# Kernel optimization log

Measured on AMD Instinct MI355X. Metric: run time of the kernel, lower is better.

Reference implementation:

```python
import jax, jax.numpy as jnp
import numpy as np

B, N_MM, N_V, N_A = 2, 256, 64, 128
DIM, HEADS, ATTN_RATIO, MLP_RATIO = 1024, 16, 0.25, 4.0
INNER = int(DIM * ATTN_RATIO)          # 256
HID = int(DIM * MLP_RATIO)             # 4096
SCALE = (DIM // HEADS) ** -0.5         # faithful to source: uses dim//num_heads
EPS = 1e-5


def setup_inputs() -> dict:
    key = jax.random.key(0)
    ks = jax.random.split(key, 16)
    s = 0.02
    return {
        "xmm": jax.random.normal(ks[0], (B, N_MM, DIM), jnp.float32),
        "xv": jax.random.normal(ks[1], (B, N_V, DIM), jnp.float32),
        "xa": jax.random.normal(ks[2], (B, N_A, DIM), jnp.float32),
        "ln_mm_w": jnp.ones((DIM,), jnp.float32),
        "ln_mm_b": jnp.zeros((DIM,), jnp.float32),
        "ln_v_w": jnp.ones((DIM,), jnp.float32),
        "ln_v_b": jnp.zeros((DIM,), jnp.float32),
        "ln_a_w": jnp.ones((DIM,), jnp.float32),
        "ln_a_b": jnp.zeros((DIM,), jnp.float32),
        "Wq": jax.random.normal(ks[3], (DIM, INNER), jnp.float32) * s,
        "Wkv": jax.random.normal(ks[4], (2 * DIM, 2 * INNER), jnp.float32) * s,
        "Wproj": jax.random.normal(ks[5], (INNER, DIM), jnp.float32) * s,
        "bproj": jnp.zeros((DIM,), jnp.float32),
        "ln_mlp_w": jnp.ones((DIM,), jnp.float32),
        "ln_mlp_b": jnp.zeros((DIM,), jnp.float32),
        "W1": jax.random.normal(ks[6], (DIM, HID), jnp.float32) * s,
        "b1": jnp.zeros((HID,), jnp.float32),
        "W2": jax.random.normal(ks[7], (HID, DIM), jnp.float32) * s,
        "b2": jnp.zeros((DIM,), jnp.float32),
    }


def _ln(x, w, b):
    m = x.mean(-1, keepdims=True)
    v = ((x - m) ** 2).mean(-1, keepdims=True)
    return (x - m) / jnp.sqrt(v + EPS) * w + b


def reference(xmm, xv, xa, ln_mm_w, ln_mm_b, ln_v_w, ln_v_b, ln_a_w, ln_a_b,
              Wq, Wkv, Wproj, bproj, ln_mlp_w, ln_mlp_b, W1, b1, W2, b2):
    hd = INNER // HEADS
    src_mm = _ln(xmm, ln_mm_w, ln_mm_b)
    src_v = _ln(xv, ln_v_w, ln_v_b)
    src_a = _ln(xa, ln_a_w, ln_a_b)

    # kv(x_va) where x_va = cat([xv broadcast over N_a, xa broadcast over N_v], -1).
    # Equivalent to projecting each stream separately and broadcast-adding:
    kv_v = src_v @ Wkv[:DIM]            # [B, N_v, 2*INNER]
    kv_a = src_a @ Wkv[DIM:]            # [B, N_a, 2*INNER]
    kv = kv_v[:, :, None, :] + kv_a[:, None, :, :]          # [B, N_v, N_a, 2*INNER]
    kv = kv.reshape(B, N_V * N_A, 2, HEADS, hd)
    k = kv[:, :, 0].transpose(0, 2, 1, 3)                   # [B, H, N_va, hd]
    v = kv[:, :, 1].transpose(0, 2, 1, 3)

    q = (src_mm @ Wq).reshape(B, N_MM, HEADS, hd).transpose(0, 2, 1, 3)

    attn = jnp.einsum('bhqd,bhkd->bhqk', q, k) * SCALE
    attn = jax.nn.softmax(attn, axis=-1)
    out = jnp.einsum('bhqk,bhkd->bhqd', attn, v)
    out = out.transpose(0, 2, 1, 3).reshape(B, N_MM, INNER)
    out = out @ Wproj + bproj

    xmm = xmm + out
    h = _ln(xmm, ln_mlp_w, ln_mlp_b)
    h = jax.nn.gelu(h @ W1 + b1, approximate=False) @ W2 + b2
    return xmm + h
```

## Files before the change

kernel.cpp:

```cpp
#include <hip/hip_runtime.h>
#include <hip/hip_bf16.h>
#include <math.h>


typedef unsigned short ushort_t;
typedef __attribute__((ext_vector_type(8))) __bf16 bf16x8;
typedef __attribute__((ext_vector_type(4))) float f32x4;

#define DEVFN static __device__ __forceinline__

DEVFN float bf2f(ushort_t u) {
    return __uint_as_float(((unsigned int)u) << 16);
}
DEVFN ushort_t f2bf(float f) {
    unsigned int x = __float_as_uint(f);
    unsigned int r = x + 0x7FFFu + ((x >> 16) & 1u);
    return (ushort_t)(r >> 16);
}
DEVFN void unpack8(uint4 dv, float* dst) {
    unsigned int ws[4] = {dv.x, dv.y, dv.z, dv.w};
#pragma unroll
    for (int i = 0; i < 4; i++) {
        dst[2 * i] = __uint_as_float(ws[i] << 16);
        dst[2 * i + 1] = __uint_as_float(ws[i] & 0xFFFF0000u);
    }
}

struct LNSeg {
    const float* x; const float* w; const float* b; ushort_t* out; int start;
};
struct TDesc { const float* in; ushort_t* out; int R, C, nx, start; };

__global__ __launch_bounds__(256) void prep_kernel(LNSeg l0, LNSeg l1,
                                                   LNSeg l2, TDesc d0,
                                                   TDesc d1, TDesc d2,
                                                   TDesc d3, TDesc d4,
                                                   float* stats) {
    int id = blockIdx.x;
    int tid = threadIdx.x;
    if (id == 0) ((float4*)stats)[tid] = (float4){0.f, 0.f, 0.f, 0.f};

    if (id < 896) {
        const float *x, *w, *b; ushort_t* o; int start;
        if (id >= l2.start)      { x = l2.x; w = l2.w; b = l2.b; o = l2.out; start = l2.start; }
        else if (id >= l1.start) { x = l1.x; w = l1.w; b = l1.b; o = l1.out; start = l1.start; }
        else                     { x = l0.x; w = l0.w; b = l0.b; o = l0.out; start = 0; }
        int row = id - start;
        const float4* xr4 = (const float4*)(x + (size_t)row * 1024);
        float4 v4 = xr4[tid];
        float s = v4.x + v4.y + v4.z + v4.w;
        float ss = v4.x * v4.x + v4.y * v4.y + v4.z * v4.z + v4.w * v4.w;
#pragma unroll
        for (int off = 32; off > 0; off >>= 1) {
            s += __shfl_down(s, off);
            ss += __shfl_down(ss, off);
        }
        __shared__ float red[8];
        if ((tid & 63) == 0) {
            red[tid >> 6] = s;
            red[4 + (tid >> 6)] = ss;
        }
        __syncthreads();
        s = red[0] + red[1] + red[2] + red[3];
        ss = red[4] + red[5] + red[6] + red[7];
        float mean = s * (1.f / 1024.f);
        float var = ss * (1.f / 1024.f) - mean * mean;
        float rstd = rsqrtf(var + 1e-5f);
        const float4 w4 = ((const float4*)w)[tid];
        const float4 b4 = ((const float4*)b)[tid];
        union { ushort_t u[4]; uint2 v; } pk;
        pk.u[0] = f2bf((v4.x - mean) * rstd * w4.x + b4.x);
        pk.u[1] = f2bf((v4.y - mean) * rstd * w4.y + b4.y);
        pk.u[2] = f2bf((v4.z - mean) * rstd * w4.z + b4.z);
        pk.u[3] = f2bf((v4.w - mean) * rstd * w4.w + b4.w);
        *(uint2*)(o + (size_t)row * 1024 + tid * 4) = pk.v;
        return;
    }

    int t = id - 896;
    const float* in; ushort_t* out; int R, C, nx, start;
    if (t >= d4.start)      { in = d4.in; out = d4.out; R = d4.R; C = d4.C; nx = d4.nx; start = d4.start; }
    else if (t >= d3.start) { in = d3.in; out = d3.out; R = d3.R; C = d3.C; nx = d3.nx; start = d3.start; }
    else if (t >= d2.start) { in = d2.in; out = d2.out; R = d2.R; C = d2.C; nx = d2.nx; start = d2.start; }
    else if (t >= d1.start) { in = d1.in; out = d1.out; R = d1.R; C = d1.C; nx = d1.nx; start = d1.start; }
    else                    { in = d0.in; out = d0.out; R = d0.R; C = d0.C; nx = d0.nx; start = 0; }
    int tt = t - start;
    int bx = (tt % nx) * 32;
    int by = (tt / nx) * 32;
    __shared__ ushort_t tile[32 * 33];
    int r = tid >> 3, c4 = (tid & 7) * 4;
    float4 f = *(const float4*)(in + (size_t)(by + r) * C + bx + c4);
    ushort_t* tr = tile + r * 33 + c4;
    tr[0] = f2bf(f.x); tr[1] = f2bf(f.y); tr[2] = f2bf(f.z); tr[3] = f2bf(f.w);
    __syncthreads();
    int oc = tid >> 3, or4 = (tid & 7) * 4;
    union { ushort_t u[4]; uint2 v; } pk;
#pragma unroll
    for (int j = 0; j < 4; j++) pk.u[j] = tile[(or4 + j) * 33 + oc];
    *(uint2*)(out + (size_t)(bx + oc) * R + by + or4) = pk.v;
}

DEVFN void gemm64_item(const ushort_t* __restrict__ A, int lda,
                       const ushort_t* __restrict__ B, int ldb,
                       ushort_t* __restrict__ C, int ldc, int K, int m0,
                       int n0, ushort_t* As, ushort_t* Bs) {
    constexpr int LS = 40;
    int tid = threadIdx.x;
    int wave = tid >> 6, lane = tid & 63;
    int wm = wave >> 1, wn = wave & 1;
    int quad = lane >> 4, l16 = lane & 15;

    f32x4 acc[2][2];
#pragma unroll
    for (int i = 0; i < 2; i++)
#pragma unroll
        for (int j = 0; j < 2; j++) acc[i][j] = (f32x4){0.f, 0.f, 0.f, 0.f};

    int r = tid >> 2, c = tid & 3;
    const ushort_t* Ap = A + (size_t)(m0 + r) * lda + c * 8;
    const ushort_t* Bp = B + (size_t)(n0 + r) * ldb + c * 8;
    uint4 ra = *(const uint4*)Ap;
    uint4 rb = *(const uint4*)Bp;

    for (int k0 = 0; k0 < K; k0 += 32) {
        *(uint4*)(&As[r * LS + c * 8]) = ra;
        *(uint4*)(&Bs[r * LS + c * 8]) = rb;
        __syncthreads();
        if (k0 + 32 < K) {
            ra = *(const uint4*)(Ap + k0 + 32);
            rb = *(const uint4*)(Bp + k0 + 32);
        }
        bf16x8 af[2], bfr[2];
#pragma unroll
        for (int i = 0; i < 2; i++)
            af[i] = *(const bf16x8*)(&As[(wm * 32 + i * 16 + l16) * LS + quad * 8]);
#pragma unroll
        for (int j = 0; j < 2; j++)
            bfr[j] = *(const bf16x8*)(&Bs[(wn * 32 + j * 16 + l16) * LS + quad * 8]);
#pragma unroll
        for (int i = 0; i < 2; i++)
#pragma unroll
            for (int j = 0; j < 2; j++)
                acc[i][j] = __builtin_amdgcn_mfma_f32_16x16x32_bf16(
                    af[i], bfr[j], acc[i][j], 0, 0, 0);
        __syncthreads();
    }

#pragma unroll
    for (int i = 0; i < 2; i++)
#pragma unroll
        for (int j = 0; j < 2; j++) {
            int col = n0 + wn * 32 + j * 16 + l16;
            int rbase = m0 + wm * 32 + i * 16 + quad * 4;
#pragma unroll
            for (int rr = 0; rr < 4; rr++)
                C[(size_t)(rbase + rr) * ldc + col] = f2bf(acc[i][j][rr]);
        }
}

struct GSeg {
    const ushort_t* A; const ushort_t* B; ushort_t* C;
    int lda, ldb, ldc, nx, start;
};
__global__ __launch_bounds__(256) void gemm64_multi(GSeg s0, GSeg s1, GSeg s2,
                                                    int K) {
    __shared__ ushort_t As[64 * 40];
    __shared__ ushort_t Bs[64 * 40];
    int id = blockIdx.x;
    GSeg s = (id >= s2.start) ? s2 : ((id >= s1.start) ? s1 : s0);
    int t = id - s.start;
    gemm64_item(s.A, s.lda, s.B, s.ldb, s.C, s.ldc, K, (t / s.nx) * 64,
                (t % s.nx) * 64, As, Bs);
}

template <int EPI, typename OutT>
DEVFN void gemm128_core(const ushort_t* __restrict__ A, int lda,
                        const ushort_t* __restrict__ B, int ldb,
                        OutT* __restrict__ C, int ldc,
                        const float* __restrict__ bias, int K, int m0, int n0,
                        ushort_t* As, ushort_t* Bs) {
    constexpr int LS = 40;
    int tid = threadIdx.x;
    int wave = tid >> 6, lane = tid & 63;
    int wm = wave >> 1, wn = wave & 1;
    int quad = lane >> 4, l16 = lane & 15;

    f32x4 acc[4][4];
#pragma unroll
    for (int i = 0; i < 4; i++)
#pragma unroll
        for (int j = 0; j < 4; j++) acc[i][j] = (f32x4){0.f, 0.f, 0.f, 0.f};

    int r = tid >> 1;
    int c = (tid & 1) * 16;
    const ushort_t* Ap = A + (size_t)(m0 + r) * lda + c;
    const ushort_t* Bp = B + (size_t)(n0 + r) * ldb + c;
    uint4 ra0 = *(const uint4*)Ap;
    uint4 ra1 = *(const uint4*)(Ap + 8);
    uint4 rb0 = *(const uint4*)Bp;
    uint4 rb1 = *(const uint4*)(Bp + 8);

    for (int k0 = 0; k0 < K; k0 += 32) {
        *(uint4*)(&As[r * LS + c]) = ra0;
        *(uint4*)(&As[r * LS + c + 8]) = ra1;
        *(uint4*)(&Bs[r * LS + c]) = rb0;
        *(uint4*)(&Bs[r * LS + c + 8]) = rb1;
        __syncthreads();
        if (k0 + 32 < K) {
            ra0 = *(const uint4*)(Ap + k0 + 32);
            ra1 = *(const uint4*)(Ap + k0 + 40);
            rb0 = *(const uint4*)(Bp + k0 + 32);
            rb1 = *(const uint4*)(Bp + k0 + 40);
        }
        bf16x8 af[4], bfr[4];
#pragma unroll
        for (int i = 0; i < 4; i++)
            af[i] = *(const bf16x8*)(&As[(wm * 64 + i * 16 + l16) * LS + quad * 8]);
#pragma unroll
        for (int j = 0; j < 4; j++)
            bfr[j] = *(const bf16x8*)(&Bs[(wn * 64 + j * 16 + l16) * LS + quad * 8]);
#pragma unroll
        for (int i = 0; i < 4; i++)
#pragma unroll
            for (int j = 0; j < 4; j++)
                acc[i][j] = __builtin_amdgcn_mfma_f32_16x16x32_bf16(
                    af[i], bfr[j], acc[i][j], 0, 0, 0);
        __syncthreads();
    }

#pragma unroll
    for (int i = 0; i < 4; i++)
#pragma unroll
        for (int j = 0; j < 4; j++) {
            int col = n0 + wn * 64 + j * 16 + l16;
            int rbase = m0 + wm * 64 + i * 16 + quad * 4;
            float bv = (EPI == 2) ? bias[col] : 0.f;
#pragma unroll
            for (int rr = 0; rr < 4; rr++) {
                int row = rbase + rr;
                float vv = acc[i][j][rr] + bv;
                if constexpr (EPI == 2) {
                    vv = 0.5f * vv * (1.f + erff(vv * 0.70710678118654752f));
                    C[(size_t)row * ldc + col] = (OutT)f2bf(vv);
                } else {
                    atomicAdd((float*)&C[(size_t)row * ldc + col], vv);
                }
            }
        }
}

__global__ __launch_bounds__(256) void gemm_mlp1(
    const ushort_t* __restrict__ h0, const ushort_t* __restrict__ W1t,
    const float* __restrict__ b1, ushort_t* __restrict__ g) {
    __shared__ ushort_t As[128 * 40];
    __shared__ ushort_t Bs[128 * 40];
    gemm128_core<2, ushort_t>(h0, 1024, W1t, 1024, g, 4096, b1, 1024,
                              blockIdx.y * 128, blockIdx.x * 128, As, Bs);
}

__global__ __launch_bounds__(256) void gemm_mlp2(
    const ushort_t* __restrict__ g, const ushort_t* __restrict__ W2t,
    float* __restrict__ outp) {
    __shared__ ushort_t As[128 * 40];
    __shared__ ushort_t Bs[128 * 40];
    int z = blockIdx.z;
    gemm128_core<5, float>(g + z * 512, 4096, W2t + z * 512, 4096, outp, 1024,
                           nullptr, 512, blockIdx.y * 128, blockIdx.x * 128,
                           As, Bs);
}

__global__ __launch_bounds__(256) void gemm_proj(
    const ushort_t* __restrict__ A, const ushort_t* __restrict__ Bt,
    const float* __restrict__ bproj, const float* __restrict__ xmm,
    const float* __restrict__ b2, float* __restrict__ y,
    float* __restrict__ outp, float* __restrict__ stats) {
    constexpr int LS = 40;
    __shared__ ushort_t As[64 * LS];
    __shared__ ushort_t Bs[64 * LS];
    int tid = threadIdx.x;
    int wave = tid >> 6, lane = tid & 63;
    int wm = wave >> 1, wn = wave & 1;
    int quad = lane >> 4, l16 = lane & 15;
    int m0 = blockIdx.y * 64, n0 = blockIdx.x * 64;

    f32x4 acc[2][2];
#pragma unroll
    for (int i = 0; i < 2; i++)
#pragma unroll
        for (int j = 0; j < 2; j++) acc[i][j] = (f32x4){0.f, 0.f, 0.f, 0.f};

    int r = tid >> 2, c = tid & 3;
    const ushort_t* Ap = A + (size_t)(m0 + r) * 256 + c * 8;
    const ushort_t* Bp = Bt + (size_t)(n0 + r) * 256 + c * 8;
    uint4 ra = *(const uint4*)Ap;
    uint4 rb = *(const uint4*)Bp;

    for (int k0 = 0; k0 < 256; k0 += 32) {
        *(uint4*)(&As[r * LS + c * 8]) = ra;
        *(uint4*)(&Bs[r * LS + c * 8]) = rb;
        __syncthreads();
        if (k0 + 32 < 256) {
            ra = *(const uint4*)(Ap + k0 + 32);
            rb = *(const uint4*)(Bp + k0 + 32);
        }
        bf16x8 af[2], bfr[2];
#pragma unroll
        for (int i = 0; i < 2; i++)
            af[i] = *(const bf16x8*)(&As[(wm * 32 + i * 16 + l16) * LS + quad * 8]);
#pragma unroll
        for (int j = 0; j < 2; j++)
            bfr[j] = *(const bf16x8*)(&Bs[(wn * 32 + j * 16 + l16) * LS + quad * 8]);
#pragma unroll
        for (int i = 0; i < 2; i++)
#pragma unroll
            for (int j = 0; j < 2; j++)
                acc[i][j] = __builtin_amdgcn_mfma_f32_16x16x32_bf16(
                    af[i], bfr[j], acc[i][j], 0, 0, 0);
        __syncthreads();
    }

    float rs[2][4] = {{0.f, 0.f, 0.f, 0.f}, {0.f, 0.f, 0.f, 0.f}};
    float rq[2][4] = {{0.f, 0.f, 0.f, 0.f}, {0.f, 0.f, 0.f, 0.f}};
#pragma unroll
    for (int i = 0; i < 2; i++)
#pragma unroll
        for (int j = 0; j < 2; j++) {
            int col = n0 + wn * 32 + j * 16 + l16;
            int rbase = m0 + wm * 32 + i * 16 + quad * 4;
            float bv = bproj[col];
            float b2v = b2[col];
#pragma unroll
            for (int rr = 0; rr < 4; rr++) {
                int row = rbase + rr;
                float vv = acc[i][j][rr] + bv + xmm[(size_t)row * 1024 + col];
                y[(size_t)row * 1024 + col] = vv;
                outp[(size_t)row * 1024 + col] = vv + b2v;
                rs[i][rr] += vv;
                rq[i][rr] += vv * vv;
            }
        }
#pragma unroll
    for (int i = 0; i < 2; i++)
#pragma unroll
        for (int rr = 0; rr < 4; rr++) {
            float s = rs[i][rr], q = rq[i][rr];
            s += __shfl_xor(s, 1); q += __shfl_xor(q, 1);
            s += __shfl_xor(s, 2); q += __shfl_xor(q, 2);
            s += __shfl_xor(s, 4); q += __shfl_xor(q, 4);
            s += __shfl_xor(s, 8); q += __shfl_xor(q, 8);
            if (l16 == 0) {
                int row = m0 + wm * 32 + i * 16 + quad * 4 + rr;
                atomicAdd(&stats[row], s);
                atomicAdd(&stats[512 + row], q);
            }
        }
}

__global__ __launch_bounds__(256) void ln_apply(
    const float* __restrict__ y, const float* __restrict__ stats,
    const float* __restrict__ w, const float* __restrict__ b,
    ushort_t* __restrict__ h0) {
    int row = blockIdx.x, tid = threadIdx.x;
    float s = stats[row], ss = stats[512 + row];
    float mean = s * (1.f / 1024.f);
    float rstd = rsqrtf(ss * (1.f / 1024.f) - mean * mean + 1e-5f);
    float4 v4 = ((const float4*)(y + (size_t)row * 1024))[tid];
    float4 w4 = ((const float4*)w)[tid];
    float4 b4 = ((const float4*)b)[tid];
    union { ushort_t u[4]; uint2 v; } pk;
    pk.u[0] = f2bf((v4.x - mean) * rstd * w4.x + b4.x);
    pk.u[1] = f2bf((v4.y - mean) * rstd * w4.y + b4.y);
    pk.u[2] = f2bf((v4.z - mean) * rstd * w4.z + b4.z);
    pk.u[3] = f2bf((v4.w - mean) * rstd * w4.w + b4.w);
    *(uint2*)(h0 + (size_t)row * 1024 + tid * 4) = pk.v;
}

__global__ __launch_bounds__(256) void attn_kernel(
    const ushort_t* __restrict__ q, const ushort_t* __restrict__ kvv,
    const ushort_t* __restrict__ kva, ushort_t* __restrict__ out) {
    int bh = blockIdx.x;
    int b = bh >> 4, h = bh & 15;
    int tid = threadIdx.x;

    __shared__ float Kv[64][16], Vv[64][16], Ka[128][16], Va[128][16];
    {
        int row = tid >> 2, seg = (tid >> 1) & 1, half = tid & 1;
        const ushort_t* src =
            kvv + (size_t)(b * 64 + row) * 512 + seg * 256 + h * 16 + half * 8;
        float* dst = (seg ? Vv[row] : Kv[row]) + half * 8;
        unpack8(*(const uint4*)src, dst);
    }
#pragma unroll
    for (int t2 = 0; t2 < 2; t2++) {
        int t = tid + t2 * 256;
        int row = t >> 2, seg = (t >> 1) & 1, half = t & 1;
        const ushort_t* src =
            kva + (size_t)(b * 128 + row) * 512 + seg * 256 + h * 16 + half * 8;
        float* dst = (seg ? Va[row] : Ka[row]) + half * 8;
        unpack8(*(const uint4*)src, dst);
    }
    __syncthreads();

    int qlocal = tid >> 2;
    int dg = tid & 3;
    int qrow = blockIdx.y * 64 + qlocal;
    const ushort_t* qp = q + (size_t)(b * 256 + qrow) * 256 + h * 16 + dg * 4;
    uint2 qu = *(const uint2*)qp;
    float4 qv;
    qv.x = __uint_as_float(qu.x << 16) * 0.125f;
    qv.y = __uint_as_float(qu.x & 0xFFFF0000u) * 0.125f;
    qv.z = __uint_as_float(qu.y << 16) * 0.125f;
    qv.w = __uint_as_float(qu.y & 0xFFFF0000u) * 0.125f;

    const float4* Kv4 = (const float4*)Kv;
    const float4* Vv4 = (const float4*)Vv;
    const float4* Ka4 = (const float4*)Ka;
    const float4* Va4 = (const float4*)Va;

    float4 ov = {0.f, 0.f, 0.f, 0.f};
    float den = 0.f;
#pragma unroll 8
    for (int i = 0; i < 64; i++) {
        float4 kk = Kv4[i * 4 + dg];
        float part = qv.x * kk.x + qv.y * kk.y + qv.z * kk.z + qv.w * kk.w;
        part += __shfl_xor(part, 1);
        part += __shfl_xor(part, 2);
        float pe = __expf(part);
        den += pe;
        float4 vv = Vv4[i * 4 + dg];
        ov.x += pe * vv.x; ov.y += pe * vv.y;
        ov.z += pe * vv.z; ov.w += pe * vv.w;
    }
    float4 oa = {0.f, 0.f, 0.f, 0.f};
    float dena = 0.f;
#pragma unroll 8
    for (int i = 0; i < 128; i++) {
        float4 kk = Ka4[i * 4 + dg];
        float part = qv.x * kk.x + qv.y * kk.y + qv.z * kk.z + qv.w * kk.w;
        part += __shfl_xor(part, 1);
        part += __shfl_xor(part, 2);
        float pe = __expf(part);
        dena += pe;
        float4 vv = Va4[i * 4 + dg];
        oa.x += pe * vv.x; oa.y += pe * vv.y;
        oa.z += pe * vv.z; oa.w += pe * vv.w;
    }

    float rv = 1.f / den, ra = 1.f / dena;
    union { ushort_t u[4]; uint2 v; } pk;
    pk.u[0] = f2bf(ov.x * rv + oa.x * ra);
    pk.u[1] = f2bf(ov.y * rv + oa.y * ra);
    pk.u[2] = f2bf(ov.z * rv + oa.z * ra);
    pk.u[3] = f2bf(ov.w * rv + oa.w * ra);
    *(uint2*)(out + (size_t)(b * 256 + qrow) * 256 + h * 16 + dg * 4) = pk.v;
}

extern "C" void kernel_launch(void* const* d_in, const int* in_sizes, int n_in,
                              void* d_out, int out_size, void* d_ws,
                              size_t ws_size, hipStream_t stream) {
    const float* xmm = (const float*)d_in[0];
    const float* xv = (const float*)d_in[1];
    const float* xa = (const float*)d_in[2];
    const float* ln_mm_w = (const float*)d_in[3];
    const float* ln_mm_b = (const float*)d_in[4];
    const float* ln_v_w = (const float*)d_in[5];
    const float* ln_v_b = (const float*)d_in[6];
    const float* ln_a_w = (const float*)d_in[7];
    const float* ln_a_b = (const float*)d_in[8];
    const float* Wq = (const float*)d_in[9];
    const float* Wkv = (const float*)d_in[10];
    const float* Wproj = (const float*)d_in[11];
    const float* bproj = (const float*)d_in[12];
    const float* ln_mlp_w = (const float*)d_in[13];
    const float* ln_mlp_b = (const float*)d_in[14];
    const float* W1 = (const float*)d_in[15];
    const float* b1 = (const float*)d_in[16];
    const float* W2 = (const float*)d_in[17];
    const float* b2 = (const float*)d_in[18];
    float* outp = (float*)d_out;

    char* w = (char*)d_ws;
    ushort_t* xmmN = (ushort_t*)w;    w += 512 * 1024 * 2;
    ushort_t* xvN = (ushort_t*)w;     w += 128 * 1024 * 2;
    ushort_t* xaN = (ushort_t*)w;     w += 256 * 1024 * 2;
    ushort_t* Wqt = (ushort_t*)w;     w += 256 * 1024 * 2;
    ushort_t* Wkvt = (ushort_t*)w;    w += 512 * 2048 * 2;
    ushort_t* Wprojt = (ushort_t*)w;  w += 1024 * 256 * 2;
    ushort_t* W1t = (ushort_t*)w;     w += 4096 * 1024 * 2;
    ushort_t* W2t = (ushort_t*)w;     w += 1024 * 4096 * 2;
    ushort_t* qout = (ushort_t*)w;    w += 512 * 256 * 2;
    ushort_t* kvvb = (ushort_t*)w;    w += 128 * 512 * 2;
    ushort_t* kvab = (ushort_t*)w;    w += 256 * 512 * 2;
    ushort_t* attnout = (ushort_t*)w; w += 512 * 256 * 2;
    float* y = (float*)w;             w += 512 * 1024 * 4;
    ushort_t* h0 = (ushort_t*)w;      w += 512 * 1024 * 2;
    ushort_t* g = (ushort_t*)w;       w += 512 * 4096 * 2;
    float* stats = (float*)w;         w += 1024 * 4;

    LNSeg L0{xmm, ln_mm_w, ln_mm_b, xmmN, 0};
    LNSeg L1{xv, ln_v_w, ln_v_b, xvN, 512};
    LNSeg L2{xa, ln_a_w, ln_a_b, xaN, 640};
    TDesc T0{Wq, Wqt, 1024, 256, 8, 0};
    TDesc T1{Wkv, Wkvt, 2048, 512, 16, 256};
    TDesc T2{Wproj, Wprojt, 256, 1024, 32, 1280};
    TDesc T3{W1, W1t, 1024, 4096, 128, 1536};
    TDesc T4{W2, W2t, 4096, 1024, 32, 5632};
    prep_kernel<<<896 + 9728, 256, 0, stream>>>(L0, L1, L2, T0, T1, T2, T3,
                                                T4, stats);

    GSeg G0{xmmN, Wqt, qout, 1024, 1024, 256, 4, 0};
    GSeg G1{xvN, Wkvt, kvvb, 1024, 2048, 512, 8, 32};
    GSeg G2{xaN, Wkvt + 1024, kvab, 1024, 2048, 512, 8, 48};
    gemm64_multi<<<80, 256, 0, stream>>>(G0, G1, G2, 1024);

    attn_kernel<<<dim3(32, 4), 256, 0, stream>>>(qout, kvvb, kvab, attnout);

    gemm_proj<<<dim3(16, 8), 256, 0, stream>>>(attnout, Wprojt, bproj, xmm,
                                               b2, y, outp, stats);

    ln_apply<<<512, 256, 0, stream>>>(y, stats, ln_mlp_w, ln_mlp_b, h0);

    gemm_mlp1<<<dim3(32, 4), 256, 0, stream>>>(h0, W1t, b1, g);

    gemm_mlp2<<<dim3(8, 4, 8), 256, 0, stream>>>(g, W2t, outp);

    (void)in_sizes; (void)n_in; (void)out_size; (void)ws_size;
}
```

Before: 213.9 us.

## Replace LDS-staged GEMMs with single-wave register-direct MFMA tiles

All GEMMs (qkv, proj, mlp1, mlp2) now run as one-wave blocks that load MFMA operand fragments straight from global memory into registers, with a register double buffer and no shared memory or barriers. The grids change to match: more, smaller blocks, and mlp2 uses a 4-way K split instead of 8-way. The weight transpose in the prep kernel moves from 32x32 to 64x64 tiles, so it launches far fewer blocks. The aim is to cut LDS traffic and sync overhead and raise block counts. The cost is that each wave re-reads operands from global and L2 with no sharing inside a block.

After: 207.6 us. -3.0%, faster.

```diff
diff --git a/kernel.cpp b/kernel.cpp
--- a/kernel.cpp
+++ b/kernel.cpp
@@ -17,6 +17,11 @@
     unsigned int r = x + 0x7FFFu + ((x >> 16) & 1u);
     return (ushort_t)(r >> 16);
 }
+DEVFN bf16x8 asbf8(uint4 v) {
+    union { uint4 u; bf16x8 b; } c;
+    c.u = v;
+    return c.b;
+}
 DEVFN void unpack8(uint4 dv, float* dst) {
     unsigned int ws[4] = {dv.x, dv.y, dv.z, dv.w};
 #pragma unroll
@@ -26,307 +31,116 @@
     }
 }
 
-struct LNSeg {
-    const float* x; const float* w; const float* b; ushort_t* out; int start;
-};
-struct TDesc { const float* in; ushort_t* out; int R, C, nx, start; };
-
-__global__ __launch_bounds__(256) void prep_kernel(LNSeg l0, LNSeg l1,
-                                                   LNSeg l2, TDesc d0,
-                                                   TDesc d1, TDesc d2,
-                                                   TDesc d3, TDesc d4,
-                                                   float* stats) {
+template <int TM, int K>
+DEVFN void wave_acc(const ushort_t* __restrict__ A, int lda,
+                    const ushort_t* __restrict__ B, int ldb, int m0, int n0,
+                    int lane, f32x4 (&acc)[TM][4]) {
+    int quad = lane >> 4, l16 = lane & 15;
+    const ushort_t* Ap = A + (size_t)(m0 + l16) * lda + quad * 8;
+    const ushort_t* Bp = B + (size_t)(n0 + l16) * ldb + quad * 8;
+
+    uint4 ra[TM], rb[4];
+#pragma unroll
+    for (int i = 0; i < TM; i++)
+        ra[i] = *(const uint4*)(Ap + (size_t)i * 16 * lda);
+#pragma unroll
+    for (int j = 0; j < 4; j++)
+        rb[j] = *(const uint4*)(Bp + (size_t)j * 16 * ldb);
+
+#pragma unroll 2
+    for (int k0 = 0; k0 < K; k0 += 32) {
+        uint4 na[TM], nb[4];
+        if (k0 + 32 < K) {
+#pragma unroll
+            for (int i = 0; i < TM; i++)
+                na[i] = *(const uint4*)(Ap + (size_t)i * 16 * lda + k0 + 32);
+#pragma unroll
+            for (int j = 0; j < 4; j++)
+                nb[j] = *(const uint4*)(Bp + (size_t)j * 16 * ldb + k0 + 32);
+        }
+#pragma unroll
+        for (int i = 0; i < TM; i++) {
+            bf16x8 af = asbf8(ra[i]);
+#pragma unroll
+            for (int j = 0; j < 4; j++)
+                acc[i][j] = __builtin_amdgcn_mfma_f32_16x16x32_bf16(
+                    af, asbf8(rb[j]), acc[i][j], 0, 0, 0);
+        }
+        if (k0 + 32 < K) {
+#pragma unroll
+            for (int i = 0; i < TM; i++) ra[i] = na[i];
+#pragma unroll
+            for (int j = 0; j < 4; j++) rb[j] = nb[j];
+        }
+    }
+}
+
+__global__ __launch_bounds__(64) void qkv_kernel(
+    const ushort_t* __restrict__ xmmN, const ushort_t* __restrict__ xvN,
+    const ushort_t* __restrict__ xaN, const ushort_t* __restrict__ Wqt,
+    const ushort_t* __restrict__ Wkvt, ushort_t* __restrict__ qout,
+    ushort_t* __restrict__ kvvb, ushort_t* __restrict__ kvab) {
     int id = blockIdx.x;
-    int tid = threadIdx.x;
-    if (id == 0) ((float4*)stats)[tid] = (float4){0.f, 0.f, 0.f, 0.f};
-
-    if (id < 896) {
-        const float *x, *w, *b; ushort_t* o; int start;
-        if (id >= l2.start)      { x = l2.x; w = l2.w; b = l2.b; o = l2.out; start = l2.start; }
-        else if (id >= l1.start) { x = l1.x; w = l1.w; b = l1.b; o = l1.out; start = l1.start; }
-        else                     { x = l0.x; w = l0.w; b = l0.b; o = l0.out; start = 0; }
-        int row = id - start;
-        const float4* xr4 = (const float4*)(x + (size_t)row * 1024);
-        float4 v4 = xr4[tid];
-        float s = v4.x + v4.y + v4.z + v4.w;
-        float ss = v4.x * v4.x + v4.y * v4.y + v4.z * v4.z + v4.w * v4.w;
-#pragma unroll
-        for (int off = 32; off > 0; off >>= 1) {
-            s += __shfl_down(s, off);
-            ss += __shfl_down(ss, off);
-        }
-        __shared__ float red[8];
-        if ((tid & 63) == 0) {
-            red[tid >> 6] = s;
-            red[4 + (tid >> 6)] = ss;
-        }
-        __syncthreads();
-        s = red[0] + red[1] + red[2] + red[3];
-        ss = red[4] + red[5] + red[6] + red[7];
-        float mean = s * (1.f / 1024.f);
-        float var = ss * (1.f / 1024.f) - mean * mean;
-        float rstd = rsqrtf(var + 1e-5f);
-        const float4 w4 = ((const float4*)w)[tid];
-        const float4 b4 = ((const float4*)b)[tid];
-        union { ushort_t u[4]; uint2 v; } pk;
-        pk.u[0] = f2bf((v4.x - mean) * rstd * w4.x + b4.x);
-        pk.u[1] = f2bf((v4.y - mean) * rstd * w4.y + b4.y);
-        pk.u[2] = f2bf((v4.z - mean) * rstd * w4.z + b4.z);
-        pk.u[3] = f2bf((v4.w - mean) * rstd * w4.w + b4.w);
-        *(uint2*)(o + (size_t)row * 1024 + tid * 4) = pk.v;
-        return;
-    }
-
-    int t = id - 896;
-    const float* in; ushort_t* out; int R, C, nx, start;
-    if (t >= d4.start)      { in = d4.in; out = d4.out; R = d4.R; C = d4.C; nx = d4.nx; start = d4.start; }
-    else if (t >= d3.start) { in = d3.in; out = d3.out; R = d3.R; C = d3.C; nx = d3.nx; start = d3.start; }
-    else if (t >= d2.start) { in = d2.in; out = d2.out; R = d2.R; C = d2.C; nx = d2.nx; start = d2.start; }
-    else if (t >= d1.start) { in = d1.in; out = d1.out; R = d1.R; C = d1.C; nx = d1.nx; start = d1.start; }
-    else                    { in = d0.in; out = d0.out; R = d0.R; C = d0.C; nx = d0.nx; start = 0; }
-    int tt = t - start;
-    int bx = (tt % nx) * 32;
-    int by = (tt / nx) * 32;
-    __shared__ ushort_t tile[32 * 33];
-    int r = tid >> 3, c4 = (tid & 7) * 4;
-    float4 f = *(const float4*)(in + (size_t)(by + r) * C + bx + c4);
-    ushort_t* tr = tile + r * 33 + c4;
-    tr[0] = f2bf(f.x); tr[1] = f2bf(f.y); tr[2] = f2bf(f.z); tr[3] = f2bf(f.w);
-    __syncthreads();
-    int oc = tid >> 3, or4 = (tid & 7) * 4;
-    union { ushort_t u[4]; uint2 v; } pk;
-#pragma unroll
-    for (int j = 0; j < 4; j++) pk.u[j] = tile[(or4 + j) * 33 + oc];
-    *(uint2*)(out + (size_t)(bx + oc) * R + by + or4) = pk.v;
-}
-
-DEVFN void gemm64_item(const ushort_t* __restrict__ A, int lda,
-                       const ushort_t* __restrict__ B, int ldb,
-                       ushort_t* __restrict__ C, int ldc, int K, int m0,
-                       int n0, ushort_t* As, ushort_t* Bs) {
-    constexpr int LS = 40;
-    int tid = threadIdx.x;
-    int wave = tid >> 6, lane = tid & 63;
-    int wm = wave >> 1, wn = wave & 1;
+    int lane = threadIdx.x;
+    const ushort_t *A, *B;
+    ushort_t* C;
+    int lda, ldb, ldc, m0, n0;
+    if (id < 64) {
+        A = xmmN; B = Wqt; C = qout; lda = 1024; ldb = 1024; ldc = 256;
+        m0 = (id >> 2) * 32; n0 = (id & 3) * 64;
+    } else if (id < 96) {
+        int t = id - 64;
+        A = xvN; B = Wkvt; C = kvvb; lda = 1024; ldb = 2048; ldc = 512;
+        m0 = (t >> 3) * 32; n0 = (t & 7) * 64;
+    } else {
+        int t = id - 96;
+        A = xaN; B = Wkvt + 1024; C = kvab; lda = 1024; ldb = 2048; ldc = 512;
+        m0 = (t >> 3) * 32; n0 = (t & 7) * 64;
+    }
+    f32x4 acc[2][4];
+#pragma unroll
+    for (int i = 0; i < 2; i++)
+#pragma unroll
+        for (int j = 0; j < 4; j++) acc[i][j] = (f32x4){0.f, 0.f, 0.f, 0.f};
+    wave_acc<2, 1024>(A, lda, B, ldb, m0, n0, lane, acc);
+
     int quad = lane >> 4, l16 = lane & 15;
-
-    f32x4 acc[2][2];
 #pragma unroll
     for (int i = 0; i < 2; i++)
 #pragma unroll
-        for (int j = 0; j < 2; j++) acc[i][j] = (f32x4){0.f, 0.f, 0.f, 0.f};
-
-    int r = tid >> 2, c = tid & 3;
-    const ushort_t* Ap = A + (size_t)(m0 + r) * lda + c * 8;
-    const ushort_t* Bp = B + (size_t)(n0 + r) * ldb + c * 8;
-    uint4 ra = *(const uint4*)Ap;
-    uint4 rb = *(const uint4*)Bp;
-
-    for (int k0 = 0; k0 < K; k0 += 32) {
-        *(uint4*)(&As[r * LS + c * 8]) = ra;
-        *(uint4*)(&Bs[r * LS + c * 8]) = rb;
-        __syncthreads();
-        if (k0 + 32 < K) {
-            ra = *(const uint4*)(Ap + k0 + 32);
-            rb = *(const uint4*)(Bp + k0 + 32);
-        }
-        bf16x8 af[2], bfr[2];
-#pragma unroll
-        for (int i = 0; i < 2; i++)
-            af[i] = *(const bf16x8*)(&As[(wm * 32 + i * 16 + l16) * LS + quad * 8]);
-#pragma unroll
-        for (int j = 0; j < 2; j++)
-            bfr[j] = *(const bf16x8*)(&Bs[(wn * 32 + j * 16 + l16) * LS + quad * 8]);
-#pragma unroll
-        for (int i = 0; i < 2; i++)
-#pragma unroll
-            for (int j = 0; j < 2; j++)
-                acc[i][j] = __builtin_amdgcn_mfma_f32_16x16x32_bf16(
-                    af[i], bfr[j], acc[i][j], 0, 0, 0);
-        __syncthreads();
-    }
-
-#pragma unroll
-    for (int i = 0; i < 2; i++)
-#pragma unroll
-        for (int j = 0; j < 2; j++) {
-            int col = n0 + wn * 32 + j * 16 + l16;
-            int rbase = m0 + wm * 32 + i * 16 + quad * 4;
+        for (int j = 0; j < 4; j++) {
+            int col = n0 + j * 16 + l16;
+            int rbase = m0 + i * 16 + quad * 4;
 #pragma unroll
             for (int rr = 0; rr < 4; rr++)
                 C[(size_t)(rbase + rr) * ldc + col] = f2bf(acc[i][j][rr]);
         }
 }
 
-struct GSeg {
-    const ushort_t* A; const ushort_t* B; ushort_t* C;
-    int lda, ldb, ldc, nx, start;
-};
-__global__ __launch_bounds__(256) void gemm64_multi(GSeg s0, GSeg s1, GSeg s2,
-                                                    int K) {
-    __shared__ ushort_t As[64 * 40];
-    __shared__ ushort_t Bs[64 * 40];
-    int id = blockIdx.x;
-    GSeg s = (id >= s2.start) ? s2 : ((id >= s1.start) ? s1 : s0);
-    int t = id - s.start;
-    gemm64_item(s.A, s.lda, s.B, s.ldb, s.C, s.ldc, K, (t / s.nx) * 64,
-                (t % s.nx) * 64, As, Bs);
-}
-
-template <int EPI, typename OutT>
-DEVFN void gemm128_core(const ushort_t* __restrict__ A, int lda,
-                        const ushort_t* __restrict__ B, int ldb,
-                        OutT* __restrict__ C, int ldc,
-                        const float* __restrict__ bias, int K, int m0, int n0,
-                        ushort_t* As, ushort_t* Bs) {
-    constexpr int LS = 40;
-    int tid = threadIdx.x;
-    int wave = tid >> 6, lane = tid & 63;
-    int wm = wave >> 1, wn = wave & 1;
-    int quad = lane >> 4, l16 = lane & 15;
-
-    f32x4 acc[4][4];
-#pragma unroll
-    for (int i = 0; i < 4; i++)
-#pragma unroll
-        for (int j = 0; j < 4; j++) acc[i][j] = (f32x4){0.f, 0.f, 0.f, 0.f};
-
-    int r = tid >> 1;
-    int c = (tid & 1) * 16;
-    const ushort_t* Ap = A + (size_t)(m0 + r) * lda + c;
-    const ushort_t* Bp = B + (size_t)(n0 + r) * ldb + c;
-    uint4 ra0 = *(const uint4*)Ap;
-    uint4 ra1 = *(const uint4*)(Ap + 8);
-    uint4 rb0 = *(const uint4*)Bp;
-    uint4 rb1 = *(const uint4*)(Bp + 8);
-
-    for (int k0 = 0; k0 < K; k0 += 32) {
-        *(uint4*)(&As[r * LS + c]) = ra0;
-        *(uint4*)(&As[r * LS + c + 8]) = ra1;
-        *(uint4*)(&Bs[r * LS + c]) = rb0;
-        *(uint4*)(&Bs[r * LS + c + 8]) = rb1;
-        __syncthreads();
-        if (k0 + 32 < K) {
-            ra0 = *(const uint4*)(Ap + k0 + 32);
-            ra1 = *(const uint4*)(Ap + k0 + 40);
-            rb0 = *(const uint4*)(Bp + k0 + 32);
-            rb1 = *(const uint4*)(Bp + k0 + 40);
-        }
-        bf16x8 af[4], bfr[4];
-#pragma unroll
-        for (int i = 0; i < 4; i++)
-            af[i] = *(const bf16x8*)(&As[(wm * 64 + i * 16 + l16) * LS + quad * 8]);
-#pragma unroll
-        for (int j = 0; j < 4; j++)
-            bfr[j] = *(const bf16x8*)(&Bs[(wn * 64 + j * 16 + l16) * LS + quad * 8]);
-#pragma unroll
-        for (int i = 0; i < 4; i++)
-#pragma unroll
-            for (int j = 0; j < 4; j++)
-                acc[i][j] = __builtin_amdgcn_mfma_f32_16x16x32_bf16(
-                    af[i], bfr[j], acc[i][j], 0, 0, 0);
-        __syncthreads();
-    }
-
-#pragma unroll
-    for (int i = 0; i < 4; i++)
-#pragma unroll
-        for (int j = 0; j < 4; j++) {
-            int col = n0 + wn * 64 + j * 16 + l16;
-            int rbase = m0 + wm * 64 + i * 16 + quad * 4;
-            float bv = (EPI == 2) ? bias[col] : 0.f;
-#pragma unroll
-            for (int rr = 0; rr < 4; rr++) {
-                int row = rbase + rr;
-                float vv = acc[i][j][rr] + bv;
-                if constexpr (EPI == 2) {
-                    vv = 0.5f * vv * (1.f + erff(vv * 0.70710678118654752f));
-                    C[(size_t)row * ldc + col] = (OutT)f2bf(vv);
-                } else {
-                    atomicAdd((float*)&C[(size_t)row * ldc + col], vv);
-                }
-            }
-        }
-}
-
-__global__ __launch_bounds__(256) void gemm_mlp1(
-    const ushort_t* __restrict__ h0, const ushort_t* __restrict__ W1t,
-    const float* __restrict__ b1, ushort_t* __restrict__ g) {
-    __shared__ ushort_t As[128 * 40];
-    __shared__ ushort_t Bs[128 * 40];
-    gemm128_core<2, ushort_t>(h0, 1024, W1t, 1024, g, 4096, b1, 1024,
-                              blockIdx.y * 128, blockIdx.x * 128, As, Bs);
-}
-
-__global__ __launch_bounds__(256) void gemm_mlp2(
-    const ushort_t* __restrict__ g, const ushort_t* __restrict__ W2t,
-    float* __restrict__ outp) {
-    __shared__ ushort_t As[128 * 40];
-    __shared__ ushort_t Bs[128 * 40];
-    int z = blockIdx.z;
-    gemm128_core<5, float>(g + z * 512, 4096, W2t + z * 512, 4096, outp, 1024,
-                           nullptr, 512, blockIdx.y * 128, blockIdx.x * 128,
-                           As, Bs);
-}
-
-__global__ __launch_bounds__(256) void gemm_proj(
-    const ushort_t* __restrict__ A, const ushort_t* __restrict__ Bt,
+__global__ __launch_bounds__(64) void proj_kernel(
+    const ushort_t* __restrict__ attnout, const ushort_t* __restrict__ Wprojt,
     const float* __restrict__ bproj, const float* __restrict__ xmm,
     const float* __restrict__ b2, float* __restrict__ y,
     float* __restrict__ outp, float* __restrict__ stats) {
-    constexpr int LS = 40;
-    __shared__ ushort_t As[64 * LS];
-    __shared__ ushort_t Bs[64 * LS];
-    int tid = threadIdx.x;
-    int wave = tid >> 6, lane = tid & 63;
-    int wm = wave >> 1, wn = wave & 1;
+    int id = blockIdx.x;
+    int lane = threadIdx.x;
+    int m0 = (id >> 4) * 32, n0 = (id & 15) * 64;
+    f32x4 acc[2][4];
+#pragma unroll
+    for (int i = 0; i < 2; i++)
+#pragma unroll
+        for (int j = 0; j < 4; j++) acc[i][j] = (f32x4){0.f, 0.f, 0.f, 0.f};
+    wave_acc<2, 256>(attnout, 256, Wprojt, 256, m0, n0, lane, acc);
+
     int quad = lane >> 4, l16 = lane & 15;
-    int m0 = blockIdx.y * 64, n0 = blockIdx.x * 64;
-
-    f32x4 acc[2][2];
-#pragma unroll
-    for (int i = 0; i < 2; i++)
-#pragma unroll
-        for (int j = 0; j < 2; j++) acc[i][j] = (f32x4){0.f, 0.f, 0.f, 0.f};
-
-    int r = tid >> 2, c = tid & 3;
-    const ushort_t* Ap = A + (size_t)(m0 + r) * 256 + c * 8;
-    const ushort_t* Bp = Bt + (size_t)(n0 + r) * 256 + c * 8;
-    uint4 ra = *(const uint4*)Ap;
-    uint4 rb = *(const uint4*)Bp;
-
-    for (int k0 = 0; k0 < 256; k0 += 32) {
-        *(uint4*)(&As[r * LS + c * 8]) = ra;
-        *(uint4*)(&Bs[r * LS + c * 8]) = rb;
-        __syncthreads();
-        if (k0 + 32 < 256) {
-            ra = *(const uint4*)(Ap + k0 + 32);
-            rb = *(const uint4*)(Bp + k0 + 32);
-        }
-        bf16x8 af[2], bfr[2];
-#pragma unroll
-        for (int i = 0; i < 2; i++)
-            af[i] = *(const bf16x8*)(&As[(wm * 32 + i * 16 + l16) * LS + quad * 8]);
-#pragma unroll
-        for (int j = 0; j < 2; j++)
-            bfr[j] = *(const bf16x8*)(&Bs[(wn * 32 + j * 16 + l16) * LS + quad * 8]);
-#pragma unroll
-        for (int i = 0; i < 2; i++)
-#pragma unroll
-            for (int j = 0; j < 2; j++)
-                acc[i][j] = __builtin_amdgcn_mfma_f32_16x16x32_bf16(
-                    af[i], bfr[j], acc[i][j], 0, 0, 0);
-        __syncthreads();
-    }
-
     float rs[2][4] = {{0.f, 0.f, 0.f, 0.f}, {0.f, 0.f, 0.f, 0.f}};
     float rq[2][4] = {{0.f, 0.f, 0.f, 0.f}, {0.f, 0.f, 0.f, 0.f}};
 #pragma unroll
     for (int i = 0; i < 2; i++)
 #pragma unroll
-        for (int j = 0; j < 2; j++) {
-            int col = n0 + wn * 32 + j * 16 + l16;
-            int rbase = m0 + wm * 32 + i * 16 + quad * 4;
+        for (int j = 0; j < 4; j++) {
+            int col = n0 + j * 16 + l16;
+            int rbase = m0 + i * 16 + quad * 4;
             float bv = bproj[col];
             float b2v = b2[col];
 #pragma unroll
@@ -349,10 +163,69 @@
             s += __shfl_xor(s, 4); q += __shfl_xor(q, 4);
             s += __shfl_xor(s, 8); q += __shfl_xor(q, 8);
             if (l16 == 0) {
-                int row = m0 + wm * 32 + i * 16 + quad * 4 + rr;
+                int row = m0 + i * 16 + quad * 4 + rr;
                 atomicAdd(&stats[row], s);
                 atomicAdd(&stats[512 + row], q);
             }
+        }
+}
+
+__global__ __launch_bounds__(64) void mlp1_kernel(
+    const ushort_t* __restrict__ h0, const ushort_t* __restrict__ W1t,
+    const float* __restrict__ b1, ushort_t* __restrict__ g) {
+    int id = blockIdx.x;
+    int lane = threadIdx.x;
+    int m0 = (id >> 6) * 64, n0 = (id & 63) * 64;
+    f32x4 acc[4][4];
+#pragma unroll
+    for (int i = 0; i < 4; i++)
+#pragma unroll
+        for (int j = 0; j < 4; j++) acc[i][j] = (f32x4){0.f, 0.f, 0.f, 0.f};
+    wave_acc<4, 1024>(h0, 1024, W1t, 1024, m0, n0, lane, acc);
+
+    int quad = lane >> 4, l16 = lane & 15;
+#pragma unroll
+    for (int i = 0; i < 4; i++)
+#pragma unroll
+        for (int j = 0; j < 4; j++) {
+            int col = n0 + j * 16 + l16;
+            int rbase = m0 + i * 16 + quad * 4;
+            float bv = b1[col];
+#pragma unroll
+            for (int rr = 0; rr < 4; rr++) {
+                float vv = acc[i][j][rr] + bv;
+                vv = 0.5f * vv * (1.f + erff(vv * 0.70710678118654752f));
+                g[(size_t)(rbase + rr) * 4096 + col] = f2bf(vv);
+            }
+        }
+}
+
+__global__ __launch_bounds__(64) void mlp2_kernel(
+    const ushort_t* __restrict__ g, const ushort_t* __restrict__ W2t,
+    float* __restrict__ outp) {
+    int id = blockIdx.x;
+    int z = blockIdx.y;
+    int lane = threadIdx.x;
+    int m0 = (id >> 4) * 64, n0 = (id & 15) * 64;
+    f32x4 acc[4][4];
+#pragma unroll
+    for (int i = 0; i < 4; i++)
+#pragma unroll
+        for (int j = 0; j < 4; j++) acc[i][j] = (f32x4){0.f, 0.f, 0.f, 0.f};
+    wave_acc<4, 1024>(g + z * 1024, 4096, W2t + z * 1024, 4096, m0, n0, lane,
+                      acc);
+
+    int quad = lane >> 4, l16 = lane & 15;
+#pragma unroll
+    for (int i = 0; i < 4; i++)
+#pragma unroll
+        for (int j = 0; j < 4; j++) {
+            int col = n0 + j * 16 + l16;
+            int rbase = m0 + i * 16 + quad * 4;
+#pragma unroll
+            for (int rr = 0; rr < 4; rr++)
+                atomicAdd(&outp[(size_t)(rbase + rr) * 1024 + col],
+                          acc[i][j][rr]);
         }
 }
 
@@ -373,6 +246,88 @@
     pk.u[2] = f2bf((v4.z - mean) * rstd * w4.z + b4.z);
     pk.u[3] = f2bf((v4.w - mean) * rstd * w4.w + b4.w);
     *(uint2*)(h0 + (size_t)row * 1024 + tid * 4) = pk.v;
+}
+
+struct LNSeg {
+    const float* x; const float* w; const float* b; ushort_t* out; int start;
+};
+struct TDesc { const float* in; ushort_t* out; int R, C, nx, start; };
+
+__global__ __launch_bounds__(256) void prep_kernel(LNSeg l0, LNSeg l1,
+                                                   LNSeg l2, TDesc d0,
+                                                   TDesc d1, TDesc d2,
+                                                   TDesc d3, TDesc d4,
+                                                   float* stats) {
+    int id = blockIdx.x;
+    int tid = threadIdx.x;
+    if (id == 0) ((float4*)stats)[tid] = (float4){0.f, 0.f, 0.f, 0.f};
+
+    if (id < 896) {
+        const float *x, *w, *b; ushort_t* o; int start;
+        if (id >= l2.start)      { x = l2.x; w = l2.w; b = l2.b; o = l2.out; start = l2.start; }
+        else if (id >= l1.start) { x = l1.x; w = l1.w; b = l1.b; o = l1.out; start = l1.start; }
+        else                     { x = l0.x; w = l0.w; b = l0.b; o = l0.out; start = 0; }
+        int row = id - start;
+        const float4* xr4 = (const float4*)(x + (size_t)row * 1024);
+        float4 v4 = xr4[tid];
+        float s = v4.x + v4.y + v4.z + v4.w;
+        float ss = v4.x * v4.x + v4.y * v4.y + v4.z * v4.z + v4.w * v4.w;
+#pragma unroll
+        for (int off = 32; off > 0; off >>= 1) {
+            s += __shfl_down(s, off);
+            ss += __shfl_down(ss, off);
+        }
+        __shared__ float red[8];
+        if ((tid & 63) == 0) {
+            red[tid >> 6] = s;
+            red[4 + (tid >> 6)] = ss;
+        }
+        __syncthreads();
+        s = red[0] + red[1] + red[2] + red[3];
+        ss = red[4] + red[5] + red[6] + red[7];
+        float mean = s * (1.f / 1024.f);
+        float var = ss * (1.f / 1024.f) - mean * mean;
+        float rstd = rsqrtf(var + 1e-5f);
+        const float4 w4 = ((const float4*)w)[tid];
+        const float4 b4 = ((const float4*)b)[tid];
+        union { ushort_t u[4]; uint2 v; } pk;
+        pk.u[0] = f2bf((v4.x - mean) * rstd * w4.x + b4.x);
+        pk.u[1] = f2bf((v4.y - mean) * rstd * w4.y + b4.y);
+        pk.u[2] = f2bf((v4.z - mean) * rstd * w4.z + b4.z);
+        pk.u[3] = f2bf((v4.w - mean) * rstd * w4.w + b4.w);
+        *(uint2*)(o + (size_t)row * 1024 + tid * 4) = pk.v;
+        return;
+    }
+
+    int t = id - 896;
+    const float* in; ushort_t* out; int R, C, nx, start;
+    if (t >= d4.start)      { in = d4.in; out = d4.out; R = d4.R; C = d4.C; nx = d4.nx; start = d4.start; }
+    else if (t >= d3.start) { in = d3.in; out = d3.out; R = d3.R; C = d3.C; nx = d3.nx; start = d3.start; }
+    else if (t >= d2.start) { in = d2.in; out = d2.out; R = d2.R; C = d2.C; nx = d2.nx; start = d2.start; }
+    else if (t >= d1.start) { in = d1.in; out = d1.out; R = d1.R; C = d1.C; nx = d1.nx; start = d1.start; }
+    else                    { in = d0.in; out = d0.out; R = d0.R; C = d0.C; nx = d0.nx; start = 0; }
+    int tt = t - start;
+    int bx = (tt % nx) * 64;
+    int by = (tt / nx) * 64;
+    __shared__ ushort_t tile[64 * 65];
+    int r = tid >> 4, c4 = (tid & 15) * 4;
+#pragma unroll
+    for (int rr = 0; rr < 4; rr++) {
+        int rl = r + rr * 16;
+        float4 f = *(const float4*)(in + (size_t)(by + rl) * C + bx + c4);
+        ushort_t* tr = tile + rl * 65 + c4;
+        tr[0] = f2bf(f.x); tr[1] = f2bf(f.y);
+        tr[2] = f2bf(f.z); tr[3] = f2bf(f.w);
+    }
+    __syncthreads();
+#pragma unroll
+    for (int rr = 0; rr < 4; rr++) {
+        int orow = r + rr * 16;
+        union { ushort_t u[4]; uint2 v; } pk;
+#pragma unroll
+        for (int j = 0; j < 4; j++) pk.u[j] = tile[(c4 + j) * 65 + orow];
+        *(uint2*)(out + (size_t)(bx + orow) * R + by + c4) = pk.v;
+    }
 }
 
 __global__ __launch_bounds__(256) void attn_kernel(
@@ -500,29 +455,27 @@
     LNSeg L0{xmm, ln_mm_w, ln_mm_b, xmmN, 0};
     LNSeg L1{xv, ln_v_w, ln_v_b, xvN, 512};
     LNSeg L2{xa, ln_a_w, ln_a_b, xaN, 640};
-    TDesc T0{Wq, Wqt, 1024, 256, 8, 0};
-    TDesc T1{Wkv, Wkvt, 2048, 512, 16, 256};
-    TDesc T2{Wproj, Wprojt, 256, 1024, 32, 1280};
-    TDesc T3{W1, W1t, 1024, 4096, 128, 1536};
-    TDesc T4{W2, W2t, 4096, 1024, 32, 5632};
-    prep_kernel<<<896 + 9728, 256, 0, stream>>>(L0, L1, L2, T0, T1, T2, T3,
+    TDesc T0{Wq, Wqt, 1024, 256, 4, 0};
+    TDesc T1{Wkv, Wkvt, 2048, 512, 8, 64};
+    TDesc T2{Wproj, Wprojt, 256, 1024, 16, 320};
+    TDesc T3{W1, W1t, 1024, 4096, 64, 384};
+    TDesc T4{W2, W2t, 4096, 1024, 16, 1408};
+    prep_kernel<<<896 + 2432, 256, 0, stream>>>(L0, L1, L2, T0, T1, T2, T3,
                                                 T4, stats);
 
-    GSeg G0{xmmN, Wqt, qout, 1024, 1024, 256, 4, 0};
-    GSeg G1{xvN, Wkvt, kvvb, 1024, 2048, 512, 8, 32};
-    GSeg G2{xaN, Wkvt + 1024, kvab, 1024, 2048, 512, 8, 48};
-    gemm64_multi<<<80, 256, 0, stream>>>(G0, G1, G2, 1024);
+    qkv_kernel<<<160, 64, 0, stream>>>(xmmN, xvN, xaN, Wqt, Wkvt, qout, kvvb,
+                                       kvab);
 
     attn_kernel<<<dim3(32, 4), 256, 0, stream>>>(qout, kvvb, kvab, attnout);
 
-    gemm_proj<<<dim3(16, 8), 256, 0, stream>>>(attnout, Wprojt, bproj, xmm,
-                                               b2, y, outp, stats);
+    proj_kernel<<<256, 64, 0, stream>>>(attnout, Wprojt, bproj, xmm, b2, y,
+                                        outp, stats);
 
     ln_apply<<<512, 256, 0, stream>>>(y, stats, ln_mlp_w, ln_mlp_b, h0);
 
-    gemm_mlp1<<<dim3(32, 4), 256, 0, stream>>>(h0, W1t, b1, g);
-
-    gemm_mlp2<<<dim3(8, 4, 8), 256, 0, stream>>>(g, W2t, outp);
+    mlp1_kernel<<<512, 64, 0, stream>>>(h0, W1t, b1, g);
+
+    mlp2_kernel<<<dim3(128, 4), 64, 0, stream>>>(g, W2t, outp);
 
     (void)in_sizes; (void)n_in; (void)out_size; (void)ws_size;
 }
```
